# Performance work log

Measured on AMD Instinct MI355X. Metric: run time of the kernel, lower is better.

Reference implementation:

```python
import jax, jax.numpy as jnp
import numpy as np

B, S, D, H = 8, 1024, 512, 8
HD = D // H
EPS = 1e-5


def layer_norm(x, g, b):
    m = jnp.mean(x, axis=-1, keepdims=True)
    v = jnp.mean(jnp.square(x - m), axis=-1, keepdims=True)
    return (x - m) * jax.lax.rsqrt(v + EPS) * g + b


def mha(x, w_in, b_in, w_out, b_out):
    # x: [B,S,D]; w_in: [3D,D]; PyTorch MultiheadAttention math (no dropout, eval)
    b, s, d = x.shape
    qkv = x @ w_in.T + b_in                      # [B,S,3D]
    q, k, v = jnp.split(qkv, 3, axis=-1)
    q = q.reshape(b, s, H, HD)
    k = k.reshape(b, s, H, HD)
    v = v.reshape(b, s, H, HD)
    scores = jnp.einsum('bqhd,bkhd->bhqk', q, k) / np.sqrt(HD)
    a = jax.nn.softmax(scores, axis=-1)
    o = jnp.einsum('bhqk,bkhd->bqhd', a, v).reshape(b, s, d)
    return o @ w_out.T + b_out


def interp_linear(y, out_size):
    # y: [B,S_in,D]; torch F.interpolate(mode='linear', align_corners=False)
    s_in = y.shape[1]
    scale = s_in / out_size
    src = (jnp.arange(out_size, dtype=jnp.float32) + 0.5) * scale - 0.5
    src = jnp.clip(src, 0.0, s_in - 1.0)
    i0 = jnp.floor(src).astype(jnp.int32)
    i1 = jnp.minimum(i0 + 1, s_in - 1)
    w = (src - i0.astype(jnp.float32))[None, :, None]
    return y[:, i0, :] * (1.0 - w) + y[:, i1, :] * w


def setup_inputs() -> dict:
    key = jax.random.key(0)
    ks = jax.random.split(key, 16)
    sd = 0.02
    return {
        'x': jax.random.normal(ks[0], (B, S, D), jnp.float32),
        'w_in1': jax.random.normal(ks[1], (3 * D, D), jnp.float32) * sd,
        'b_in1': jnp.zeros((3 * D,), jnp.float32),
        'w_out1': jax.random.normal(ks[2], (D, D), jnp.float32) * sd,
        'b_out1': jnp.zeros((D,), jnp.float32),
        'w_in2': jax.random.normal(ks[3], (3 * D, D), jnp.float32) * sd,
        'b_in2': jnp.zeros((3 * D,), jnp.float32),
        'w_out2': jax.random.normal(ks[4], (D, D), jnp.float32) * sd,
        'b_out2': jnp.zeros((D,), jnp.float32),
        'g1': jnp.ones((D,), jnp.float32), 'beta1': jnp.zeros((D,), jnp.float32),
        'g2': jnp.ones((D,), jnp.float32), 'beta2': jnp.zeros((D,), jnp.float32),
        'g3': jnp.ones((D,), jnp.float32), 'beta3': jnp.zeros((D,), jnp.float32),
        'w_ff1': jax.random.normal(ks[5], (4 * D, D), jnp.float32) * sd,
        'b_ff1': jnp.zeros((4 * D,), jnp.float32),
        'w_ff2': jax.random.normal(ks[6], (D, 4 * D), jnp.float32) * sd,
        'b_ff2': jnp.zeros((D,), jnp.float32),
    }


def reference(x, w_in1, b_in1, w_out1, b_out1, w_in2, b_in2, w_out2, b_out2,
              g1, beta1, g2, beta2, g3, beta3, w_ff1, b_ff1, w_ff2, b_ff2):
    a1 = mha(x, w_in1, b_in1, w_out1, b_out1)
    x = layer_norm(x + a1, g1, beta1)
    # avg_pool1d kernel=2 stride=2 ceil_mode (S even -> exact halving)
    pooled = x.reshape(B, S // 2, 2, D).mean(axis=2)
    a2 = mha(pooled, w_in2, b_in2, w_out2, b_out2)
    up = interp_linear(a2, S)
    x = layer_norm(x + up, g2, beta2)
    h = jax.nn.gelu(x @ w_ff1.T + b_ff1, approximate=False)
    ff = h @ w_ff2.T + b_ff2
    return layer_norm(x + ff, g3, beta3)
```

## Files before the change

### kernel.cpp

```cpp
#include <hip/hip_runtime.h>
#include <hip/hip_bf16.h>
#include <math.h>

typedef __hip_bfloat16 bf16;
typedef __attribute__((ext_vector_type(8))) short short8;
typedef __attribute__((ext_vector_type(4))) float f32x4;
typedef __attribute__((ext_vector_type(16))) float f32x16;

__device__ __forceinline__ float ldf(const float* p, size_t i) { return p[i]; }
__device__ __forceinline__ float ldf(const bf16*  p, size_t i) { return __bfloat162float(p[i]); }
__device__ __forceinline__ void  stf(float* p, size_t i, float v) { p[i] = v; }
__device__ __forceinline__ void  stf(bf16*  p, size_t i, float v) { p[i] = __float2bfloat16(v); }

__device__ __forceinline__ float ex2(float x) { return __builtin_amdgcn_exp2f(x); }

__device__ __forceinline__ void gl16(const void* gp, void* lp) {
    __builtin_amdgcn_global_load_lds(
        (const __attribute__((address_space(1))) void*)gp,
        (__attribute__((address_space(3))) void*)lp, 16, 0, 0);
}

__device__ __forceinline__ void pl32swap(unsigned &a, unsigned &b) {
    asm volatile("v_permlane32_swap_b32 %0, %1" : "+v"(a), "+v"(b));
}

__global__ __launch_bounds__(256) void cvt_kernel(
    const float* __restrict__ src, bf16* __restrict__ dst, int n)
{
    for (int i = blockIdx.x * 256 + threadIdx.x; i < n; i += gridDim.x * 256)
        dst[i] = __float2bfloat16(src[i]);
}

__global__ __launch_bounds__(256) void cvt_w(
    const float* __restrict__ s0, const float* __restrict__ s1,
    const float* __restrict__ s2, const float* __restrict__ s3,
    const float* __restrict__ s4, const float* __restrict__ s5,
    bf16* __restrict__ dst)
{
    int i = blockIdx.x * 256 + threadIdx.x;
    const float* s; int off;
    if      (i <  786432) { s = s0; off = 0; }
    else if (i < 1048576) { s = s1; off =  786432; }
    else if (i < 1835008) { s = s2; off = 1048576; }
    else if (i < 2097152) { s = s3; off = 1835008; }
    else if (i < 3145728) { s = s4; off = 2097152; }
    else                  { s = s5; off = 3145728; }
    dst[i] = __float2bfloat16(s[i - off]);
}

template <int EPI, int BN, int VS>
__global__ __launch_bounds__(256) void gemm_rs(
    const bf16* __restrict__ A, const bf16* __restrict__ W,
    const float* __restrict__ bias, bf16* __restrict__ C,
    bf16* __restrict__ vt, int M, int N, int K)
{
    constexpr int WNC = BN / 2;
    constexpr int NT  = BN / 32;
    constexpr int RB  = BN / 32;

    __shared__ __align__(16) bf16 Asl[2][128 * 64];
    __shared__ __align__(16) bf16 Bsl[2][BN * 64];

    const int tid  = threadIdx.x;
    const int lane = tid & 63;
    const int wave = tid >> 6;
    const int wm   = wave >> 1, wn = wave & 1;
    const int l15  = lane & 15, quad = lane >> 4;

    const int nwg = gridDim.x * gridDim.y;
    const int bid = blockIdx.y * gridDim.x + blockIdx.x;
    const int wid = (bid & 7) * (nwg >> 3) + (bid >> 3);
    const int bx  = wid % gridDim.x, by = wid / gridDim.x;
    const int row0 = by * 128, col0 = bx * BN;

    const int sr = tid >> 3;
    const int gg = tid & 7;

    const bf16* As[4]; const bf16* Ws[RB]; int loA[4], loB[RB];
    #pragma unroll
    for (int j = 0; j < 4; j++) {
        int row = j * 32 + sr;
        int gs  = (gg ^ (row & 7)) * 8;
        As[j]  = &A[(size_t)(row0 + row) * K + gs];
        loA[j] = row * 64 + gg * 8;
    }
    #pragma unroll
    for (int j = 0; j < RB; j++) {
        int row = j * 32 + sr;
        int gs  = (gg ^ (row & 7)) * 8;
        Ws[j]  = &W[(size_t)(col0 + row) * K + gs];
        loB[j] = row * 64 + gg * 8;
    }

    short8 ga[4], gb[RB];
    auto LOADG = [&](int k0) {
        #pragma unroll
        for (int j = 0; j < 4; j++) ga[j] = *(const short8*)(As[j] + k0);
        #pragma unroll
        for (int j = 0; j < RB; j++) gb[j] = *(const short8*)(Ws[j] + k0);
    };
    auto WRITEL = [&](int buf) {
        #pragma unroll
        for (int j = 0; j < 4; j++) *(short8*)&Asl[buf][loA[j]] = ga[j];
        #pragma unroll
        for (int j = 0; j < RB; j++) *(short8*)&Bsl[buf][loB[j]] = gb[j];
    };

    f32x4 acc[4][NT] = {};
    const int nk = K >> 6;

    LOADG(0);
    WRITEL(0);
    __syncthreads();

    int cur = 0;
    for (int i = 0; i < nk; i++) {
        if (i + 1 < nk) LOADG((i + 1) << 6);

        #pragma unroll
        for (int ks = 0; ks < 64; ks += 32) {
            short8 af[4], bfr[NT];
            const int g0 = (ks >> 3) + quad;
            const int col = (g0 ^ (l15 & 7)) * 8;
            #pragma unroll
            for (int mt = 0; mt < 4; mt++)
                af[mt] = *(const short8*)&Asl[cur][(wm * 64 + mt * 16 + l15) * 64 + col];
            #pragma unroll
            for (int nt = 0; nt < NT; nt++)
                bfr[nt] = *(const short8*)&Bsl[cur][(wn * WNC + nt * 16 + l15) * 64 + col];
            #pragma unroll
            for (int mt = 0; mt < 4; mt++)
                #pragma unroll
                for (int nt = 0; nt < NT; nt++)
                    acc[mt][nt] = __builtin_amdgcn_mfma_f32_16x16x32_bf16(
                        af[mt], bfr[nt], acc[mt][nt], 0, 0, 0);
        }

        if (i + 1 < nk) WRITEL(cur ^ 1);
        __syncthreads();
        cur ^= 1;
    }

    if constexpr (VS > 0) {
        if (col0 >= 1024) {
            constexpr int LS = (VS == 1024) ? 10 : 9;
            #pragma unroll
            for (int mt = 0; mt < 4; mt++) {
                int rowm = row0 + wm * 64 + mt * 16 + quad * 4;
                int b8 = rowm >> LS;
                int s4 = rowm & (VS - 1);
                #pragma unroll
                for (int nt = 0; nt < NT; nt++) {
                    int col = col0 + wn * WNC + nt * 16 + l15;
                    float bv = bias[col];
                    int hd = col - 1024;
                    union { bf16 b4[4]; unsigned long long u; } pk;
                    #pragma unroll
                    for (int r = 0; r < 4; r++)
                        pk.b4[r] = __float2bfloat16(acc[mt][nt][r] + bv);
                    *(unsigned long long*)&vt[
                        ((size_t)(b8 * 8 + (hd >> 6)) * 64 + (hd & 63)) * VS + s4] = pk.u;
                }
            }
            return;
        }
    }

    #pragma unroll
    for (int mt = 0; mt < 4; mt++) {
        int row = row0 + wm * 64 + mt * 16 + quad * 4;
        #pragma unroll
        for (int nt = 0; nt < NT; nt++) {
            int col = col0 + wn * WNC + nt * 16 + l15;
            float bv = bias[col];
            #pragma unroll
            for (int r = 0; r < 4; r++) {
                float v = acc[mt][nt][r] + bv;
                if (EPI == 1) v = 0.5f * v * (1.0f + erff(v * 0.70710678118654752f));
                C[(size_t)(row + r) * N + col] = __float2bfloat16(v);
            }
        }
    }
}

template <int LQB>
__global__ __launch_bounds__(128) void flash_attn_mfma(
    const bf16* __restrict__ qkv, const bf16* __restrict__ vt,
    bf16* __restrict__ o)
{
    constexpr int S  = 64 << LQB;
    constexpr int nt = 1 << LQB;

    __shared__ __align__(16) bf16 Kl[2][64 * 64];

    const int tid  = threadIdx.x;
    const int wave = tid >> 6, lane = tid & 63;
    const int l31  = lane & 31, hi = lane >> 5;

    const int r    = blockIdx.x;
    const int w    = (r & 7) * ((1 << LQB) * 8) + (r >> 3);
    const int qblk = w & ((1 << LQB) - 1);
    const int bh   = w >> LQB;
    const int h    = bh & 7, bb = bh >> 3;
    const int q0   = qblk * 64 + wave * 32;

    const bf16* base  = qkv + (size_t)bb * S * 1536 + h * 64;
    const bf16* vbase = vt + (size_t)bh * 64 * S;

    short8 qf[4];
    #pragma unroll
    for (int c = 0; c < 4; c++)
        qf[c] = *(const short8*)&base[(size_t)(q0 + l31) * 1536 + c * 16 + hi * 8];

    const int sr = lane >> 3;
    const int sc = ((lane & 7) ^ sr) * 8;

    auto STGK = [&](int buf, int k0) {
        #pragma unroll
        for (int t = 0; t < 4; t++) {
            int r0 = wave * 32 + t * 8;
            gl16(&base[(size_t)(k0 + r0 + sr) * 1536 + 512 + sc], &Kl[buf][r0 * 64]);
        }
    };

    f32x16 oacc[2] = {};
    float lrow = 0.f;
    const float CE = 0.18033688f;

    STGK(0, 0);

    for (int it = 0; it < nt; it++) {
        const int cur = it & 1;
        __syncthreads();
        if (it + 1 < nt) STGK(cur ^ 1, (it + 1) << 6);

        short8 vf[2][2][2];
        {
            const bf16* vb = vbase + (it << 6) + hi * 8;
            #pragma unroll
            for (int dt = 0; dt < 2; dt++) {
                const bf16* vd = &vb[(size_t)(dt * 32 + l31) * S];
                #pragma unroll
                for (int sub = 0; sub < 2; sub++)
                    #pragma unroll
                    for (int kk = 0; kk < 2; kk++)
                        vf[sub][kk][dt] = *(const short8*)&vd[sub * 32 + kk * 16];
            }
        }

        const bf16* Kc = &Kl[cur][0];
        #pragma unroll
        for (int sub = 0; sub < 2; sub++) {
            f32x16 st = {};
            #pragma unroll
            for (int c = 0; c < 4; c++) {
                const int row  = sub * 32 + l31;
                const int slot = (c * 2 + hi) ^ (row & 7);
                short8 af = *(const short8*)&Kc[row * 64 + slot * 8];
                st = __builtin_amdgcn_mfma_f32_32x32x16_bf16(af, qf[c], st, 0, 0, 0);
            }

            float p[16]; float ps = 0.f;
            #pragma unroll
            for (int r2 = 0; r2 < 16; r2++) {
                p[r2] = ex2(st[r2] * CE - 2.0f);
                ps += p[r2];
            }
            lrow += ps;

            unsigned wk[8];
            #pragma unroll
            for (int j = 0; j < 8; j++)
                asm("v_cvt_pk_bf16_f32 %0, %1, %2" : "=v"(wk[j]) : "v"(p[2*j]), "v"(p[2*j+1]));

            #pragma unroll
            for (int kk = 0; kk < 2; kk++) {
                pl32swap(wk[kk*4+0], wk[kk*4+2]);
                pl32swap(wk[kk*4+1], wk[kk*4+3]);
                union { unsigned u[4]; short8 s; } pa;
                pa.u[0] = wk[kk*4+0]; pa.u[1] = wk[kk*4+1];
                pa.u[2] = wk[kk*4+2]; pa.u[3] = wk[kk*4+3];
                #pragma unroll
                for (int dt = 0; dt < 2; dt++)
                    oacc[dt] = __builtin_amdgcn_mfma_f32_32x32x16_bf16(
                        pa.s, vf[sub][kk][dt], oacc[dt], 0, 0, 0);
            }
        }
    }

    lrow += __shfl_xor(lrow, 32);
    float inv = 1.0f / lrow;
    #pragma unroll
    for (int r2 = 0; r2 < 16; r2++) {
        int qr = (r2 & 3) + 8 * (r2 >> 2) + 4 * hi;
        float iv = __shfl(inv, qr);
        size_t rb = ((size_t)bb * S + q0 + qr) * 512 + h * 64;
        o[rb + l31]      = __float2bfloat16(oacc[0][r2] * iv);
        o[rb + 32 + l31] = __float2bfloat16(oacc[1][r2] * iv);
    }
}

template <typename AT, typename OT, bool INTERP>
__global__ __launch_bounds__(256) void ln_kernel(
    const AT* __restrict__ a, const bf16* __restrict__ bsrc,
    const float* __restrict__ g, const float* __restrict__ beta,
    OT* __restrict__ out)
{
    const int row = blockIdx.x;
    const int t = threadIdx.x;
    const size_t base = (size_t)row * 512;

    float a0 = ldf(a, base + t), a1 = ldf(a, base + t + 256);
    float b0, b1;
    if (INTERP) {
        int s = row & 1023, bb = row >> 10;
        float src = fminf(fmaxf((s + 0.5f) * 0.5f - 0.5f, 0.f), 511.f);
        int i0 = (int)src;
        int i1 = min(i0 + 1, 511);
        float w = src - (float)i0;
        size_t r0 = ((size_t)bb * 512 + i0) * 512;
        size_t r1 = ((size_t)bb * 512 + i1) * 512;
        b0 = __bfloat162float(bsrc[r0 + t]) * (1.f - w) + __bfloat162float(bsrc[r1 + t]) * w;
        b1 = __bfloat162float(bsrc[r0 + t + 256]) * (1.f - w) + __bfloat162float(bsrc[r1 + t + 256]) * w;
    } else {
        b0 = __bfloat162float(bsrc[base + t]);
        b1 = __bfloat162float(bsrc[base + t + 256]);
    }
    float v0 = a0 + b0, v1 = a1 + b1;

    __shared__ float red[4];
    const int lane = t & 63, wid = t >> 6;

    float sm = v0 + v1;
    #pragma unroll
    for (int off = 32; off > 0; off >>= 1) sm += __shfl_xor(sm, off);
    if (lane == 0) red[wid] = sm;
    __syncthreads();
    sm = red[0] + red[1] + red[2] + red[3];
    const float mean = sm * (1.0f / 512.0f);

    float d0 = v0 - mean, d1 = v1 - mean;
    float vv = d0 * d0 + d1 * d1;
    __syncthreads();
    #pragma unroll
    for (int off = 32; off > 0; off >>= 1) vv += __shfl_xor(vv, off);
    if (lane == 0) red[wid] = vv;
    __syncthreads();
    vv = red[0] + red[1] + red[2] + red[3];
    const float rstd = rsqrtf(vv * (1.0f / 512.0f) + 1e-5f);

    stf(out, base + t,       d0 * rstd * g[t]       + beta[t]);
    stf(out, base + t + 256, d1 * rstd * g[t + 256] + beta[t + 256]);
}

__global__ __launch_bounds__(256) void ln_pool_kernel(
    const float* __restrict__ a, const bf16* __restrict__ bsrc,
    const float* __restrict__ g, const float* __restrict__ beta,
    bf16* __restrict__ x1, bf16* __restrict__ pooled)
{
    const int pr = blockIdx.x;
    const int t = threadIdx.x;
    const size_t base0 = (size_t)(2 * pr) * 512;
    const size_t base1 = base0 + 512;

    float u0 = a[base0 + t]       + __bfloat162float(bsrc[base0 + t]);
    float u1 = a[base0 + t + 256] + __bfloat162float(bsrc[base0 + t + 256]);
    float w0 = a[base1 + t]       + __bfloat162float(bsrc[base1 + t]);
    float w1 = a[base1 + t + 256] + __bfloat162float(bsrc[base1 + t + 256]);

    __shared__ float red[2][4];
    const int lane = t & 63, wid = t >> 6;

    float s0 = u0 + u1, s1 = w0 + w1;
    #pragma unroll
    for (int off = 32; off > 0; off >>= 1) {
        s0 += __shfl_xor(s0, off);
        s1 += __shfl_xor(s1, off);
    }
    if (lane == 0) { red[0][wid] = s0; red[1][wid] = s1; }
    __syncthreads();
    const float m0 = (red[0][0] + red[0][1] + red[0][2] + red[0][3]) * (1.0f / 512.0f);
    const float m1 = (red[1][0] + red[1][1] + red[1][2] + red[1][3]) * (1.0f / 512.0f);

    float du0 = u0 - m0, du1 = u1 - m0, dw0 = w0 - m1, dw1 = w1 - m1;
    float v0 = du0 * du0 + du1 * du1, v1 = dw0 * dw0 + dw1 * dw1;
    __syncthreads();
    #pragma unroll
    for (int off = 32; off > 0; off >>= 1) {
        v0 += __shfl_xor(v0, off);
        v1 += __shfl_xor(v1, off);
    }
    if (lane == 0) { red[0][wid] = v0; red[1][wid] = v1; }
    __syncthreads();
    const float r0 = rsqrtf((red[0][0] + red[0][1] + red[0][2] + red[0][3]) * (1.0f / 512.0f) + 1e-5f);
    const float r1 = rsqrtf((red[1][0] + red[1][1] + red[1][2] + red[1][3]) * (1.0f / 512.0f) + 1e-5f);

    float g0 = g[t], g1v = g[t + 256], be0 = beta[t], be1 = beta[t + 256];
    float y00 = du0 * r0 * g0  + be0;
    float y01 = du1 * r0 * g1v + be1;
    float y10 = dw0 * r1 * g0  + be0;
    float y11 = dw1 * r1 * g1v + be1;

    x1[base0 + t]       = __float2bfloat16(y00);
    x1[base0 + t + 256] = __float2bfloat16(y01);
    x1[base1 + t]       = __float2bfloat16(y10);
    x1[base1 + t + 256] = __float2bfloat16(y11);

    const size_t pb = (size_t)pr * 512;
    pooled[pb + t]       = __float2bfloat16(0.5f * (y00 + y10));
    pooled[pb + t + 256] = __float2bfloat16(0.5f * (y01 + y11));
}

extern "C" void kernel_launch(void* const* d_in, const int* in_sizes, int n_in,
                              void* d_out, int out_size, void* d_ws, size_t ws_size,
                              hipStream_t stream)
{
    const float* x      = (const float*)d_in[0];
    const float* w_in1  = (const float*)d_in[1];
    const float* b_in1  = (const float*)d_in[2];
    const float* w_out1 = (const float*)d_in[3];
    const float* b_out1 = (const float*)d_in[4];
    const float* w_in2  = (const float*)d_in[5];
    const float* b_in2  = (const float*)d_in[6];
    const float* w_out2 = (const float*)d_in[7];
    const float* b_out2 = (const float*)d_in[8];
    const float* g1     = (const float*)d_in[9];
    const float* be1    = (const float*)d_in[10];
    const float* g2     = (const float*)d_in[11];
    const float* be2    = (const float*)d_in[12];
    const float* g3     = (const float*)d_in[13];
    const float* be3    = (const float*)d_in[14];
    const float* w_ff1  = (const float*)d_in[15];
    const float* b_ff1  = (const float*)d_in[16];
    const float* w_ff2  = (const float*)d_in[17];
    const float* b_ff2  = (const float*)d_in[18];

    bf16* ws     = (bf16*)d_ws;
    bf16* xb     = ws + 0;
    bf16* wq1    = ws + 4194304;
    bf16* wo1    = ws + 4980736;
    bf16* wq2    = ws + 5242880;
    bf16* wo2    = ws + 6029312;
    bf16* wf1    = ws + 6291456;
    bf16* wf2    = ws + 7340032;
    bf16* qkv1   = ws + 8388608;
    bf16* o1     = ws + 20971520;
    bf16* a1     = ws + 25165824;
    bf16* x1     = ws + 29360128;
    bf16* pooled = ws + 33554432;
    bf16* qkv2   = ws + 35651584;
    bf16* o2     = ws + 41943040;
    bf16* a2     = ws + 44040192;
    bf16* x2     = ws + 46137344;
    bf16* h      = ws + 8388608;
    bf16* ff     = ws + 25165824;
    bf16* vt     = ws + 46137344;

    dim3 blk(256);
    dim3 fblk(128);

    cvt_kernel<<<4096, blk, 0, stream>>>(x, xb, 4194304);
    cvt_w<<<16384, blk, 0, stream>>>(w_in1, w_out1, w_in2, w_out2, w_ff1, w_ff2, wq1);

    gemm_rs<0,128,1024><<<dim3(12, 64), blk, 0, stream>>>(xb, wq1, b_in1, qkv1, vt, 8192, 1536, 512);
    flash_attn_mfma<4><<<dim3(1024), fblk, 0, stream>>>(qkv1, vt, o1);
    gemm_rs<0,64,0><<<dim3(8, 64), blk, 0, stream>>>(o1, wo1, b_out1, a1, nullptr, 8192, 512, 512);
    ln_pool_kernel<<<4096, blk, 0, stream>>>(x, a1, g1, be1, x1, pooled);
    gemm_rs<0,64,512><<<dim3(24, 32), blk, 0, stream>>>(pooled, wq2, b_in2, qkv2, vt, 4096, 1536, 512);
    flash_attn_mfma<3><<<dim3(512), fblk, 0, stream>>>(qkv2, vt, o2);
    gemm_rs<0,64,0><<<dim3(8, 32), blk, 0, stream>>>(o2, wo2, b_out2, a2, nullptr, 4096, 512, 512);
    ln_kernel<bf16, bf16, true><<<8192, blk, 0, stream>>>(x1, a2, g2, be2, x2);
    gemm_rs<1,128,0><<<dim3(16, 64), blk, 0, stream>>>(x2, wf1, b_ff1, h, nullptr, 8192, 2048, 512);
    gemm_rs<0,64,0><<<dim3(8, 64), blk, 0, stream>>>(h, wf2, b_ff2, ff, nullptr, 8192, 512, 2048);
    ln_kernel<bf16, float, false><<<8192, blk, 0, stream>>>(x2, ff, g3, be3, (float*)d_out);
}
```

Before: 311.7 us.

## Split attention key loop across two wave pairs with LDS reduction

The flash attention kernel now launches 256 threads. Two wave pairs each process alternating 64-key tiles for the same 32-row query slices, and their partial output accumulators and row sums are combined through LDS at the end. This doubles the waves per block to hide latency, and wraps the MFMA sections in s_setprio. The costs are twice the K shared memory, an extra reduction and sync at the end, and higher register pressure under the 256-thread launch bound. The softmax uses a fixed offset rather than a running max, so partials sum directly.

```diff
diff --git a/kernel.cpp b/kernel.cpp
--- a/kernel.cpp
+++ b/kernel.cpp
@@ -184,25 +184,27 @@
 }
 
 template <int LQB>
-__global__ __launch_bounds__(128) void flash_attn_mfma(
+__global__ __launch_bounds__(256) void flash_attn_mfma(
     const bf16* __restrict__ qkv, const bf16* __restrict__ vt,
     bf16* __restrict__ o)
 {
-    constexpr int S  = 64 << LQB;
-    constexpr int nt = 1 << LQB;
-
-    __shared__ __align__(16) bf16 Kl[2][64 * 64];
+    constexpr int S   = 64 << LQB;
+    constexpr int nt2 = 1 << (LQB - 1);
+
+    __shared__ __align__(16) bf16 Kl[2][2][64 * 64];
 
     const int tid  = threadIdx.x;
     const int wave = tid >> 6, lane = tid & 63;
     const int l31  = lane & 31, hi = lane >> 5;
+    const int wq   = wave & 1;
+    const int wp   = wave >> 1;
 
     const int r    = blockIdx.x;
     const int w    = (r & 7) * ((1 << LQB) * 8) + (r >> 3);
     const int qblk = w & ((1 << LQB) - 1);
     const int bh   = w >> LQB;
     const int h    = bh & 7, bb = bh >> 3;
-    const int q0   = qblk * 64 + wave * 32;
+    const int q0   = qblk * 64 + wq * 32;
 
     const bf16* base  = qkv + (size_t)bb * S * 1536 + h * 64;
     const bf16* vbase = vt + (size_t)bh * 64 * S;
@@ -215,11 +217,18 @@
     const int sr = lane >> 3;
     const int sc = ((lane & 7) ^ sr) * 8;
 
-    auto STGK = [&](int buf, int k0) {
+    auto STGK = [&](int buf, int j) {
+        const int t0 = 2 * j + wp;
+        #pragma unroll
+        for (int t = 0; t < 2; t++) {
+            int r0 = wq * 32 + t * 16;
+            (void)r0;
+        }
         #pragma unroll
         for (int t = 0; t < 4; t++) {
-            int r0 = wave * 32 + t * 8;
-            gl16(&base[(size_t)(k0 + r0 + sr) * 1536 + 512 + sc], &Kl[buf][r0 * 64]);
+            int r0 = wq * 32 + t * 8;
+            gl16(&base[(size_t)((t0 << 6) + r0 + sr) * 1536 + 512 + sc],
+                 &Kl[buf][wp][r0 * 64]);
         }
     };
 
@@ -229,14 +238,16 @@
 
     STGK(0, 0);
 
-    for (int it = 0; it < nt; it++) {
-        const int cur = it & 1;
+    for (int j = 0; j < nt2; j++) {
+        const int cur = j & 1;
         __syncthreads();
-        if (it + 1 < nt) STGK(cur ^ 1, (it + 1) << 6);
+        if (j + 1 < nt2) STGK(cur ^ 1, j + 1);
+
+        const int t0 = 2 * j + wp;
 
         short8 vf[2][2][2];
         {
-            const bf16* vb = vbase + (it << 6) + hi * 8;
+            const bf16* vb = vbase + (t0 << 6) + hi * 8;
             #pragma unroll
             for (int dt = 0; dt < 2; dt++) {
                 const bf16* vd = &vb[(size_t)(dt * 32 + l31) * S];
@@ -248,10 +259,11 @@
             }
         }
 
-        const bf16* Kc = &Kl[cur][0];
+        const bf16* Kc = &Kl[cur][wp][0];
         #pragma unroll
         for (int sub = 0; sub < 2; sub++) {
             f32x16 st = {};
+            __builtin_amdgcn_s_setprio(1);
             #pragma unroll
             for (int c = 0; c < 4; c++) {
                 const int row  = sub * 32 + l31;
@@ -259,6 +271,7 @@
                 short8 af = *(const short8*)&Kc[row * 64 + slot * 8];
                 st = __builtin_amdgcn_mfma_f32_32x32x16_bf16(af, qf[c], st, 0, 0, 0);
             }
+            __builtin_amdgcn_s_setprio(0);
 
             float p[16]; float ps = 0.f;
             #pragma unroll
@@ -270,9 +283,10 @@
 
             unsigned wk[8];
             #pragma unroll
-            for (int j = 0; j < 8; j++)
-                asm("v_cvt_pk_bf16_f32 %0, %1, %2" : "=v"(wk[j]) : "v"(p[2*j]), "v"(p[2*j+1]));
-
+            for (int jj = 0; jj < 8; jj++)
+                asm("v_cvt_pk_bf16_f32 %0, %1, %2" : "=v"(wk[jj]) : "v"(p[2*jj]), "v"(p[2*jj+1]));
+
+            __builtin_amdgcn_s_setprio(1);
             #pragma unroll
             for (int kk = 0; kk < 2; kk++) {
                 pl32swap(wk[kk*4+0], wk[kk*4+2]);
@@ -285,18 +299,41 @@
                     oacc[dt] = __builtin_amdgcn_mfma_f32_32x32x16_bf16(
                         pa.s, vf[sub][kk][dt], oacc[dt], 0, 0, 0);
             }
-        }
-    }
-
-    lrow += __shfl_xor(lrow, 32);
-    float inv = 1.0f / lrow;
-    #pragma unroll
-    for (int r2 = 0; r2 < 16; r2++) {
-        int qr = (r2 & 3) + 8 * (r2 >> 2) + 4 * hi;
-        float iv = __shfl(inv, qr);
-        size_t rb = ((size_t)bb * S + q0 + qr) * 512 + h * 64;
-        o[rb + l31]      = __float2bfloat16(oacc[0][r2] * iv);
-        o[rb + 32 + l31] = __float2bfloat16(oacc[1][r2] * iv);
+            __builtin_amdgcn_s_setprio(0);
+        }
+    }
+
+    __syncthreads();
+    float* fb = (float*)&Kl[0][0][0];
+    if (wp == 1) {
+        const int bi = (wq * 64 + lane) * 33;
+        #pragma unroll
+        for (int r2 = 0; r2 < 16; r2++) {
+            fb[bi + r2]      = oacc[0][r2];
+            fb[bi + 16 + r2] = oacc[1][r2];
+        }
+        fb[bi + 32] = lrow;
+    }
+    __syncthreads();
+    if (wp == 0) {
+        const int bi = (wq * 64 + lane) * 33;
+        #pragma unroll
+        for (int r2 = 0; r2 < 16; r2++) {
+            oacc[0][r2] += fb[bi + r2];
+            oacc[1][r2] += fb[bi + 16 + r2];
+        }
+        lrow += fb[bi + 32];
+
+        lrow += __shfl_xor(lrow, 32);
+        float inv = 1.0f / lrow;
+        #pragma unroll
+        for (int r2 = 0; r2 < 16; r2++) {
+            int qr = (r2 & 3) + 8 * (r2 >> 2) + 4 * hi;
+            float iv = __shfl(inv, qr);
+            size_t rb = ((size_t)bb * S + q0 + qr) * 512 + h * 64;
+            o[rb + l31]      = __float2bfloat16(oacc[0][r2] * iv);
+            o[rb + 32 + l31] = __float2bfloat16(oacc[1][r2] * iv);
+        }
     }
 }
 
@@ -457,17 +494,16 @@
     bf16* vt     = ws + 46137344;
 
     dim3 blk(256);
-    dim3 fblk(128);
 
     cvt_kernel<<<4096, blk, 0, stream>>>(x, xb, 4194304);
     cvt_w<<<16384, blk, 0, stream>>>(w_in1, w_out1, w_in2, w_out2, w_ff1, w_ff2, wq1);
 
     gemm_rs<0,128,1024><<<dim3(12, 64), blk, 0, stream>>>(xb, wq1, b_in1, qkv1, vt, 8192, 1536, 512);
-    flash_attn_mfma<4><<<dim3(1024), fblk, 0, stream>>>(qkv1, vt, o1);
+    flash_attn_mfma<4><<<dim3(1024), blk, 0, stream>>>(qkv1, vt, o1);
     gemm_rs<0,64,0><<<dim3(8, 64), blk, 0, stream>>>(o1, wo1, b_out1, a1, nullptr, 8192, 512, 512);
     ln_pool_kernel<<<4096, blk, 0, stream>>>(x, a1, g1, be1, x1, pooled);
     gemm_rs<0,64,512><<<dim3(24, 32), blk, 0, stream>>>(pooled, wq2, b_in2, qkv2, vt, 4096, 1536, 512);
-    flash_attn_mfma<3><<<dim3(512), fblk, 0, stream>>>(qkv2, vt, o2);
+    flash_attn_mfma<3><<<dim3(512), blk, 0, stream>>>(qkv2, vt, o2);
     gemm_rs<0,64,0><<<dim3(8, 32), blk, 0, stream>>>(o2, wo2, b_out2, a2, nullptr, 4096, 512, 512);
     ln_kernel<bf16, bf16, true><<<8192, blk, 0, stream>>>(x1, a2, g2, be2, x2);
     gemm_rs<1,128,0><<<dim3(16, 64), blk, 0, stream>>>(x2, wf1, b_ff1, h, nullptr, 8192, 2048, 512);
```

Result: no change. 313.6 us (+0.6%).

## Merge conversion kernels and widen flash-attention K tiles to 128 keys

Applied to the files above, without the earlier changes.

Merges the input and weight fp32-to-bf16 conversions into one launch, which assumes xb and wq1 sit next to each other in the workspace. Flash attention now stages 128 keys of K per iteration instead of 64, halving the number of barrier/prefetch rounds. It also loads twice as many V fragments into registers. s_setprio raises wave priority around the MFMA sections so the matrix work and the exp/softmax work of different waves overlap better. The cost is double the LDS per block and higher register pressure, which may reduce occupancy.

```diff
diff --git a/kernel.cpp b/kernel.cpp
--- a/kernel.cpp
+++ b/kernel.cpp
@@ -24,28 +24,27 @@
     asm volatile("v_permlane32_swap_b32 %0, %1" : "+v"(a), "+v"(b));
 }
 
-__global__ __launch_bounds__(256) void cvt_kernel(
-    const float* __restrict__ src, bf16* __restrict__ dst, int n)
-{
-    for (int i = blockIdx.x * 256 + threadIdx.x; i < n; i += gridDim.x * 256)
-        dst[i] = __float2bfloat16(src[i]);
-}
-
-__global__ __launch_bounds__(256) void cvt_w(
+__global__ __launch_bounds__(256) void cvt_all(
+    const float* __restrict__ x,
     const float* __restrict__ s0, const float* __restrict__ s1,
     const float* __restrict__ s2, const float* __restrict__ s3,
     const float* __restrict__ s4, const float* __restrict__ s5,
     bf16* __restrict__ dst)
 {
     int i = blockIdx.x * 256 + threadIdx.x;
+    if (i < 4194304) {
+        dst[i] = __float2bfloat16(x[i]);
+        return;
+    }
+    int j = i - 4194304;
     const float* s; int off;
-    if      (i <  786432) { s = s0; off = 0; }
-    else if (i < 1048576) { s = s1; off =  786432; }
-    else if (i < 1835008) { s = s2; off = 1048576; }
-    else if (i < 2097152) { s = s3; off = 1835008; }
-    else if (i < 3145728) { s = s4; off = 2097152; }
+    if      (j <  786432) { s = s0; off = 0; }
+    else if (j < 1048576) { s = s1; off =  786432; }
+    else if (j < 1835008) { s = s2; off = 1048576; }
+    else if (j < 2097152) { s = s3; off = 1835008; }
+    else if (j < 3145728) { s = s4; off = 2097152; }
     else                  { s = s5; off = 3145728; }
-    dst[i] = __float2bfloat16(s[i - off]);
+    dst[i] = __float2bfloat16(s[j - off]);
 }
 
 template <int EPI, int BN, int VS>
@@ -188,10 +187,10 @@
     const bf16* __restrict__ qkv, const bf16* __restrict__ vt,
     bf16* __restrict__ o)
 {
-    constexpr int S  = 64 << LQB;
-    constexpr int nt = 1 << LQB;
-
-    __shared__ __align__(16) bf16 Kl[2][64 * 64];
+    constexpr int S   = 64 << LQB;
+    constexpr int nt2 = 1 << (LQB - 1);
+
+    __shared__ __align__(16) bf16 Kl[2][128 * 64];
 
     const int tid  = threadIdx.x;
     const int wave = tid >> 6, lane = tid & 63;
@@ -215,11 +214,12 @@
     const int sr = lane >> 3;
     const int sc = ((lane & 7) ^ sr) * 8;
 
-    auto STGK = [&](int buf, int k0) {
-        #pragma unroll
-        for (int t = 0; t < 4; t++) {
-            int r0 = wave * 32 + t * 8;
-            gl16(&base[(size_t)(k0 + r0 + sr) * 1536 + 512 + sc], &Kl[buf][r0 * 64]);
+    auto STGK = [&](int buf, int j) {
+        #pragma unroll
+        for (int t = 0; t < 8; t++) {
+            int r0 = wave * 64 + t * 8;
+            gl16(&base[(size_t)((j << 7) + r0 + sr) * 1536 + 512 + sc],
+                 &Kl[buf][r0 * 64]);
         }
     };
 
@@ -229,61 +229,72 @@
 
     STGK(0, 0);
 
-    for (int it = 0; it < nt; it++) {
-        const int cur = it & 1;
+    for (int j = 0; j < nt2; j++) {
+        const int cur = j & 1;
         __syncthreads();
-        if (it + 1 < nt) STGK(cur ^ 1, (it + 1) << 6);
-
-        short8 vf[2][2][2];
+        if (j + 1 < nt2) STGK(cur ^ 1, j + 1);
+
+        short8 vf[2][2][2][2];
         {
-            const bf16* vb = vbase + (it << 6) + hi * 8;
+            const bf16* vb = vbase + (j << 7) + hi * 8;
             #pragma unroll
             for (int dt = 0; dt < 2; dt++) {
                 const bf16* vd = &vb[(size_t)(dt * 32 + l31) * S];
                 #pragma unroll
-                for (int sub = 0; sub < 2; sub++)
+                for (int t64 = 0; t64 < 2; t64++)
                     #pragma unroll
-                    for (int kk = 0; kk < 2; kk++)
-                        vf[sub][kk][dt] = *(const short8*)&vd[sub * 32 + kk * 16];
+                    for (int sub = 0; sub < 2; sub++)
+                        #pragma unroll
+                        for (int kk = 0; kk < 2; kk++)
+                            vf[t64][sub][kk][dt] =
+                                *(const short8*)&vd[t64 * 64 + sub * 32 + kk * 16];
             }
         }
 
-        const bf16* Kc = &Kl[cur][0];
-        #pragma unroll
-        for (int sub = 0; sub < 2; sub++) {
-            f32x16 st = {};
-            #pragma unroll
-            for (int c = 0; c < 4; c++) {
-                const int row  = sub * 32 + l31;
-                const int slot = (c * 2 + hi) ^ (row & 7);
-                short8 af = *(const short8*)&Kc[row * 64 + slot * 8];
-                st = __builtin_amdgcn_mfma_f32_32x32x16_bf16(af, qf[c], st, 0, 0, 0);
-            }
-
-            float p[16]; float ps = 0.f;
-            #pragma unroll
-            for (int r2 = 0; r2 < 16; r2++) {
-                p[r2] = ex2(st[r2] * CE - 2.0f);
-                ps += p[r2];
-            }
-            lrow += ps;
-
-            unsigned wk[8];
-            #pragma unroll
-            for (int j = 0; j < 8; j++)
-                asm("v_cvt_pk_bf16_f32 %0, %1, %2" : "=v"(wk[j]) : "v"(p[2*j]), "v"(p[2*j+1]));
-
-            #pragma unroll
-            for (int kk = 0; kk < 2; kk++) {
-                pl32swap(wk[kk*4+0], wk[kk*4+2]);
-                pl32swap(wk[kk*4+1], wk[kk*4+3]);
-                union { unsigned u[4]; short8 s; } pa;
-                pa.u[0] = wk[kk*4+0]; pa.u[1] = wk[kk*4+1];
-                pa.u[2] = wk[kk*4+2]; pa.u[3] = wk[kk*4+3];
-                #pragma unroll
-                for (int dt = 0; dt < 2; dt++)
-                    oacc[dt] = __builtin_amdgcn_mfma_f32_32x32x16_bf16(
-                        pa.s, vf[sub][kk][dt], oacc[dt], 0, 0, 0);
+        #pragma unroll
+        for (int t64 = 0; t64 < 2; t64++) {
+            const bf16* Kc = &Kl[cur][t64 * 64 * 64];
+            #pragma unroll
+            for (int sub = 0; sub < 2; sub++) {
+                f32x16 st = {};
+                __builtin_amdgcn_s_setprio(1);
+                #pragma unroll
+                for (int c = 0; c < 4; c++) {
+                    const int row  = sub * 32 + l31;
+                    const int slot = (c * 2 + hi) ^ (row & 7);
+                    short8 af = *(const short8*)&Kc[row * 64 + slot * 8];
+                    st = __builtin_amdgcn_mfma_f32_32x32x16_bf16(af, qf[c], st, 0, 0, 0);
+                }
+                __builtin_amdgcn_s_setprio(0);
+
+                float p[16]; float ps = 0.f;
+                #pragma unroll
+                for (int r2 = 0; r2 < 16; r2++) {
+                    p[r2] = ex2(st[r2] * CE - 2.0f);
+                    ps += p[r2];
+                }
+                lrow += ps;
+
+                unsigned wk[8];
+                #pragma unroll
+                for (int jj = 0; jj < 8; jj++)
+                    asm("v_cvt_pk_bf16_f32 %0, %1, %2"
+                        : "=v"(wk[jj]) : "v"(p[2*jj]), "v"(p[2*jj+1]));
+
+                __builtin_amdgcn_s_setprio(1);
+                #pragma unroll
+                for (int kk = 0; kk < 2; kk++) {
+                    pl32swap(wk[kk*4+0], wk[kk*4+2]);
+                    pl32swap(wk[kk*4+1], wk[kk*4+3]);
+                    union { unsigned u[4]; short8 s; } pa;
+                    pa.u[0] = wk[kk*4+0]; pa.u[1] = wk[kk*4+1];
+                    pa.u[2] = wk[kk*4+2]; pa.u[3] = wk[kk*4+3];
+                    #pragma unroll
+                    for (int dt = 0; dt < 2; dt++)
+                        oacc[dt] = __builtin_amdgcn_mfma_f32_32x32x16_bf16(
+                            pa.s, vf[t64][sub][kk][dt], oacc[dt], 0, 0, 0);
+                }
+                __builtin_amdgcn_s_setprio(0);
             }
         }
     }
@@ -459,8 +470,7 @@
     dim3 blk(256);
     dim3 fblk(128);
 
-    cvt_kernel<<<4096, blk, 0, stream>>>(x, xb, 4194304);
-    cvt_w<<<16384, blk, 0, stream>>>(w_in1, w_out1, w_in2, w_out2, w_ff1, w_ff2, wq1);
+    cvt_all<<<32768, blk, 0, stream>>>(x, w_in1, w_out1, w_in2, w_out2, w_ff1, w_ff2, xb);
 
     gemm_rs<0,128,1024><<<dim3(12, 64), blk, 0, stream>>>(xb, wq1, b_in1, qkv1, vt, 8192, 1536, 512);
     flash_attn_mfma<4><<<dim3(1024), fblk, 0, stream>>>(qkv1, vt, o1);
```

Result: no change. 316.0 us (+1.4%).
